# Performance work log

Measured on AMD Instinct MI355X. Metric: run time of the kernel, lower is better.

## Reference

```python
import jax, jax.numpy as jnp
import numpy as np

B, T, I, H = 256, 512, 300, 128


def setup_inputs() -> dict:
    key = jax.random.key(0)
    ks = jax.random.split(key, 7)
    s_ih = 1.0 / np.sqrt(H)
    return {
        "x": jax.random.normal(ks[0], (B, T, I), dtype=jnp.float32),
        # PyTorch LSTM params, gate order i,f,g,o stacked along first axis
        "W_ih": jax.random.uniform(ks[1], (4 * H, I), minval=-s_ih, maxval=s_ih, dtype=jnp.float32),
        "W_hh": jax.random.uniform(ks[2], (4 * H, H), minval=-s_ih, maxval=s_ih, dtype=jnp.float32),
        "b_ih": jax.random.uniform(ks[3], (4 * H,), minval=-s_ih, maxval=s_ih, dtype=jnp.float32),
        "b_hh": jax.random.uniform(ks[4], (4 * H,), minval=-s_ih, maxval=s_ih, dtype=jnp.float32),
        "fc_w": jax.random.uniform(ks[5], (1, H), minval=-s_ih, maxval=s_ih, dtype=jnp.float32),
        "fc_b": jax.random.uniform(ks[6], (1,), minval=-s_ih, maxval=s_ih, dtype=jnp.float32),
    }


def _lstm_last_h(x, W_ih, W_hh, b_ih, b_hh):
    # Precompute input contributions for all timesteps at once: [B,T,4H]
    xg = jnp.einsum("bti,gi->btg", x, W_ih) + b_ih + b_hh
    xg = jnp.transpose(xg, (1, 0, 2))  # [T,B,4H] for scan

    def step(carry, xg_t):
        h, c = carry
        gates = xg_t + h @ W_hh.T  # [B,4H]
        i, f, g, o = jnp.split(gates, 4, axis=-1)
        i = jax.nn.sigmoid(i)
        f = jax.nn.sigmoid(f)
        g = jnp.tanh(g)
        o = jax.nn.sigmoid(o)
        c = f * c + i * g
        h = o * jnp.tanh(c)
        return (h, c), None

    h0 = jnp.zeros((x.shape[0], W_hh.shape[1]), dtype=x.dtype)
    (h_last, _), _ = jax.lax.scan(step, (h0, h0), xg)
    return h_last  # [B,H]


def reference(x, W_ih, W_hh, b_ih, b_hh, fc_w, fc_b):
    h_last = _lstm_last_h(x, W_ih, W_hh, b_ih, b_hh)
    return h_last @ fc_w.T + fc_b  # [B,1]
```

## Files before the change

### kernel.cpp

```cpp
#include <hip/hip_runtime.h>
#include <cstdint>
#include <cstddef>

#define Bb   256
#define Tt   512
#define Ii   300
#define Hh   128
#define G4   512
#define KP   320
#define Mm   (Bb*Tt)

typedef _Float16 h2v   __attribute__((ext_vector_type(2)));
typedef _Float16 half8 __attribute__((ext_vector_type(8)));
typedef float    f32x4 __attribute__((ext_vector_type(4)));

static __device__ __forceinline__ h2v as_h2(unsigned int u){ union{unsigned int u; h2v h;} c; c.u=u; return c.h; }
static __device__ __forceinline__ unsigned int as_u32(h2v h){ union{unsigned int u; h2v h;} c; c.h=h; return c.u; }

#if __has_builtin(__builtin_amdgcn_fdot2)
#define FDOT2(a,b,c) __builtin_amdgcn_fdot2((a),(b),(c),false)
#else
static __device__ __forceinline__ float FDOT2(h2v a, h2v b, float c){
  return c + (float)a[0]*(float)b[0] + (float)a[1]*(float)b[1];
}
#endif

__global__ __launch_bounds__(256) void conv_x(const float* __restrict__ x, unsigned int* __restrict__ x16){
  int idx = blockIdx.x*256 + threadIdx.x;
  int r   = idx / 160;
  int kk2 = idx - r*160;
  int kk  = kk2*2;
  const float* xr = x + (size_t)r*Ii;
  float v0 = (kk   < Ii) ? xr[kk]   : 0.f;
  float v1 = (kk+1 < Ii) ? xr[kk+1] : 0.f;
  h2v h; h[0] = (_Float16)v0; h[1] = (_Float16)v1;
  x16[idx] = as_u32(h);
}

__global__ __launch_bounds__(256) void conv_small(const float* __restrict__ Wih, const float* __restrict__ Whh,
      const float* __restrict__ bih, const float* __restrict__ bhh,
      unsigned int* __restrict__ W16, unsigned int* __restrict__ Whh2, float* __restrict__ bias){
  int idx = blockIdx.x*256 + threadIdx.x;
  if (idx < G4*160){
    int r = idx/160, kk2 = idx - r*160, kk = kk2*2;
    const float* wr = Wih + (size_t)r*Ii;
    float v0 = (kk   < Ii) ? wr[kk]   : 0.f;
    float v1 = (kk+1 < Ii) ? wr[kk+1] : 0.f;
    h2v h; h[0]=(_Float16)v0; h[1]=(_Float16)v1;
    W16[idx] = as_u32(h);
  } else if (idx < G4*160 + G4*64){
    int t = idx - G4*160; int j = t>>6, kk = t&63;
    float v0 = Whh[j*Hh + kk*2], v1 = Whh[j*Hh + kk*2 + 1];
    h2v h; h[0]=(_Float16)v0; h[1]=(_Float16)v1;
    Whh2[t] = as_u32(h);
  } else if (idx < G4*160 + G4*64 + G4){
    int d = idx - (G4*160 + G4*64);
    bias[d] = bih[d] + bhh[d];
  }
}

__global__ __launch_bounds__(256,2) void gemm16(const _Float16* __restrict__ A, const _Float16* __restrict__ Bm,
       const float* __restrict__ bias, float* __restrict__ C){
  __shared__ _Float16 As[128][32];
  __shared__ _Float16 Bs[128][32];
  int tid = threadIdx.x;
  int w = tid>>6, lane = tid&63;
  int bm = blockIdx.x*128, bn = blockIdx.y*128;
  f32x4 acc[2][8];
  #pragma unroll
  for (int i=0;i<2;i++)
    #pragma unroll
    for (int j=0;j<8;j++) acc[i][j] = (f32x4){0.f,0.f,0.f,0.f};

  int srow = tid>>1, scol = (tid&1)*16;
  const uint4* ga = (const uint4*)(A  + (size_t)(bm+srow)*KP + scol);
  const uint4* gb = (const uint4*)(Bm + (size_t)(bn+srow)*KP + scol);

  int q = lane>>4, mr = lane&15;
  int m0 = w*32;

  for (int kt=0; kt<KP/32; ++kt){
    __syncthreads();
    uint4 va0 = ga[0], va1 = ga[1];
    uint4 vb0 = gb[0], vb1 = gb[1];
    *(uint4*)&As[srow][scol]   = va0; *(uint4*)&As[srow][scol+8] = va1;
    *(uint4*)&Bs[srow][scol]   = vb0; *(uint4*)&Bs[srow][scol+8] = vb1;
    ga += 4; gb += 4;
    __syncthreads();
    half8 af0 = *(const half8*)&As[m0 + mr][q*8];
    half8 af1 = *(const half8*)&As[m0 + 16 + mr][q*8];
    #pragma unroll
    for (int j=0;j<8;j++){
      half8 bf = *(const half8*)&Bs[j*16 + mr][q*8];
      acc[0][j] = __builtin_amdgcn_mfma_f32_16x16x32_f16(af0, bf, acc[0][j], 0,0,0);
      acc[1][j] = __builtin_amdgcn_mfma_f32_16x16x32_f16(af1, bf, acc[1][j], 0,0,0);
    }
  }
  #pragma unroll
  for (int j=0;j<8;j++){
    int gc = bn + j*16 + mr;
    float bv = bias[gc];
    #pragma unroll
    for (int i=0;i<2;i++){
      int gr0 = bm + w*32 + i*16 + q*4;
      #pragma unroll
      for (int reg=0; reg<4; ++reg)
        C[(size_t)(gr0+reg)*G4 + gc] = acc[i][j][reg] + bv;
    }
  }
}

__global__ __launch_bounds__(256,1) void lstm_rec(const float* __restrict__ xg, const unsigned int* __restrict__ Whh2,
     const float* __restrict__ fcw, const float* __restrict__ fcb, float* __restrict__ out){
  int tid = threadIdx.x;
  int b = blockIdx.x;
  h2v w0[64], w1[64];
  #pragma unroll
  for (int kk=0; kk<64; ++kk){
    w0[kk] = as_h2(Whh2[tid*64 + kk]);
    w1[kk] = as_h2(Whh2[(tid+256)*64 + kk]);
  }
  __shared__ __align__(16) unsigned short hsh[128];
  __shared__ float2 fo_sh[128];
  __shared__ float red[256];
  if (tid < 128) hsh[tid] = 0;
  float creg = 0.f, hreg = 0.f;
  const float* xrow = xg + (size_t)b * (Tt*G4);
  float xc0 = xrow[tid], xc1 = xrow[256+tid];
  __syncthreads();

  for (int t=0; t<Tt; ++t){
    float xn0 = 0.f, xn1 = 0.f;
    if (t < Tt-1){ const float* xr = xrow + (size_t)(t+1)*G4; xn0 = xr[tid]; xn1 = xr[256+tid]; }
    float a0 = xc0, a1 = xc1;
    const uint4* hv = (const uint4*)hsh;
    #pragma unroll
    for (int kq=0; kq<16; ++kq){
      uint4 hq = hv[kq];
      h2v p0 = as_h2(hq.x), p1 = as_h2(hq.y), p2 = as_h2(hq.z), p3 = as_h2(hq.w);
      a0 = FDOT2(p0, w0[kq*4+0], a0); a1 = FDOT2(p0, w1[kq*4+0], a1);
      a0 = FDOT2(p1, w0[kq*4+1], a0); a1 = FDOT2(p1, w1[kq*4+1], a1);
      a0 = FDOT2(p2, w0[kq*4+2], a0); a1 = FDOT2(p2, w1[kq*4+2], a1);
      a0 = FDOT2(p3, w0[kq*4+3], a0); a1 = FDOT2(p3, w1[kq*4+3], a1);
    }
    if (tid >= 128){
      float f = 1.f/(1.f+__expf(-a0));
      float o = 1.f/(1.f+__expf(-a1));
      fo_sh[tid-128] = make_float2(f,o);
    }
    __syncthreads();
    if (tid < 128){
      float ig = 1.f/(1.f+__expf(-a0));
      float eg = __expf(2.f*a1); float g = 1.f - 2.f/(eg+1.f);
      float2 fo = fo_sh[tid];
      creg = fo.x*creg + ig*g;
      float ec = __expf(2.f*creg); float tc = 1.f - 2.f/(ec+1.f);
      hreg = fo.y*tc;
      union { _Float16 f; unsigned short s; } cv; cv.f = (_Float16)hreg;
      hsh[tid] = cv.s;
    }
    __syncthreads();
    xc0 = xn0; xc1 = xn1;
  }

  red[tid] = (tid < 128) ? hreg*fcw[tid] : 0.f;
  __syncthreads();
  for (int s=128; s>=1; s>>=1){
    if (tid < s) red[tid] += red[tid+s];
    __syncthreads();
  }
  if (tid == 0) out[b] = red[0] + fcb[0];
}

extern "C" void kernel_launch(void* const* d_in, const int* in_sizes, int n_in,
                              void* d_out, int out_size, void* d_ws, size_t ws_size,
                              hipStream_t stream){
  const float* x   = (const float*)d_in[0];
  const float* Wih = (const float*)d_in[1];
  const float* Whh = (const float*)d_in[2];
  const float* bih = (const float*)d_in[3];
  const float* bhh = (const float*)d_in[4];
  const float* fcw = (const float*)d_in[5];
  const float* fcb = (const float*)d_in[6];
  float* out = (float*)d_out;
  char* ws = (char*)d_ws;

  unsigned int* x16   = (unsigned int*)(ws);
  unsigned int* W16   = (unsigned int*)(ws + 83886080);
  unsigned int* Whh2w = (unsigned int*)(ws + 84213760);
  float*        bias  = (float*)      (ws + 84344832);
  float*        xg    = (float*)      (ws + 84346880);

  hipLaunchKernelGGL(conv_x,     dim3(81920),  dim3(256), 0, stream, x, x16);
  hipLaunchKernelGGL(conv_small, dim3(450),    dim3(256), 0, stream, Wih, Whh, bih, bhh, W16, Whh2w, bias);
  hipLaunchKernelGGL(gemm16,     dim3(1024,4), dim3(256), 0, stream,
                     (const _Float16*)x16, (const _Float16*)W16, bias, xg);
  hipLaunchKernelGGL(lstm_rec,   dim3(256),    dim3(256), 0, stream, xg, Whh2w, fcw, fcb, out);
}
```

Before: 708.0 us.

## Use one thread per gate row in LSTM recurrence with 512-thread blocks

```diff
diff --git a/kernel.cpp b/kernel.cpp
--- a/kernel.cpp
+++ b/kernel.cpp
@@ -110,62 +110,59 @@
   }
 }
 
-__global__ __launch_bounds__(256,1) void lstm_rec(const float* __restrict__ xg, const unsigned int* __restrict__ Whh2,
+__global__ __launch_bounds__(512,2) void lstm_rec(const float* __restrict__ xg, const unsigned int* __restrict__ Whh2,
      const float* __restrict__ fcw, const float* __restrict__ fcb, float* __restrict__ out){
   int tid = threadIdx.x;
   int b = blockIdx.x;
-  h2v w0[64], w1[64];
+  int d = tid & 127, g = tid >> 7;
+  h2v w[64];
   #pragma unroll
-  for (int kk=0; kk<64; ++kk){
-    w0[kk] = as_h2(Whh2[tid*64 + kk]);
-    w1[kk] = as_h2(Whh2[(tid+256)*64 + kk]);
-  }
+  for (int kk=0; kk<64; ++kk) w[kk] = as_h2(Whh2[tid*64 + kk]);
+
   __shared__ __align__(16) unsigned short hsh[128];
-  __shared__ float2 fo_sh[128];
-  __shared__ float red[256];
+  __shared__ __align__(16) float gsh[512];
+  __shared__ float red[128];
   if (tid < 128) hsh[tid] = 0;
   float creg = 0.f, hreg = 0.f;
   const float* xrow = xg + (size_t)b * (Tt*G4);
-  float xc0 = xrow[tid], xc1 = xrow[256+tid];
+  float xc = xrow[tid];
   __syncthreads();
 
   for (int t=0; t<Tt; ++t){
-    float xn0 = 0.f, xn1 = 0.f;
-    if (t < Tt-1){ const float* xr = xrow + (size_t)(t+1)*G4; xn0 = xr[tid]; xn1 = xr[256+tid]; }
-    float a0 = xc0, a1 = xc1;
+    float xn = 0.f;
+    if (t < Tt-1) xn = xrow[(size_t)(t+1)*G4 + tid];
+    float a0 = xc, a1 = 0.f;
     const uint4* hv = (const uint4*)hsh;
     #pragma unroll
-    for (int kq=0; kq<16; ++kq){
-      uint4 hq = hv[kq];
-      h2v p0 = as_h2(hq.x), p1 = as_h2(hq.y), p2 = as_h2(hq.z), p3 = as_h2(hq.w);
-      a0 = FDOT2(p0, w0[kq*4+0], a0); a1 = FDOT2(p0, w1[kq*4+0], a1);
-      a0 = FDOT2(p1, w0[kq*4+1], a0); a1 = FDOT2(p1, w1[kq*4+1], a1);
-      a0 = FDOT2(p2, w0[kq*4+2], a0); a1 = FDOT2(p2, w1[kq*4+2], a1);
-      a0 = FDOT2(p3, w0[kq*4+3], a0); a1 = FDOT2(p3, w1[kq*4+3], a1);
+    for (int kq=0; kq<8; ++kq){
+      uint4 hq0 = hv[kq*2], hq1 = hv[kq*2+1];
+      a0 = FDOT2(as_h2(hq0.x), w[kq*8+0], a0); a1 = FDOT2(as_h2(hq0.y), w[kq*8+1], a1);
+      a0 = FDOT2(as_h2(hq0.z), w[kq*8+2], a0); a1 = FDOT2(as_h2(hq0.w), w[kq*8+3], a1);
+      a0 = FDOT2(as_h2(hq1.x), w[kq*8+4], a0); a1 = FDOT2(as_h2(hq1.y), w[kq*8+5], a1);
+      a0 = FDOT2(as_h2(hq1.z), w[kq*8+6], a0); a1 = FDOT2(as_h2(hq1.w), w[kq*8+7], a1);
     }
-    if (tid >= 128){
-      float f = 1.f/(1.f+__expf(-a0));
-      float o = 1.f/(1.f+__expf(-a1));
-      fo_sh[tid-128] = make_float2(f,o);
+    float a = a0 + a1;
+    float act;
+    if (g == 2){ float e = __expf(2.f*a); act = 1.f - 2.f/(e+1.f); }
+    else       { act = 1.f/(1.f+__expf(-a)); }
+    gsh[d*4+g] = act;
+    __syncthreads();
+    float4 gv = *(const float4*)&gsh[d*4];
+    creg = gv.y*creg + gv.x*gv.z;
+    float ec = __expf(2.f*creg); float tc = 1.f - 2.f/(ec+1.f);
+    hreg = gv.w*tc;
+    if (g == 0){
+      union{ _Float16 f; unsigned short s; } cv; cv.f = (_Float16)hreg;
+      hsh[d] = cv.s;
     }
     __syncthreads();
-    if (tid < 128){
-      float ig = 1.f/(1.f+__expf(-a0));
-      float eg = __expf(2.f*a1); float g = 1.f - 2.f/(eg+1.f);
-      float2 fo = fo_sh[tid];
-      creg = fo.x*creg + ig*g;
-      float ec = __expf(2.f*creg); float tc = 1.f - 2.f/(ec+1.f);
-      hreg = fo.y*tc;
-      union { _Float16 f; unsigned short s; } cv; cv.f = (_Float16)hreg;
-      hsh[tid] = cv.s;
-    }
-    __syncthreads();
-    xc0 = xn0; xc1 = xn1;
+    xc = xn;
   }
 
-  red[tid] = (tid < 128) ? hreg*fcw[tid] : 0.f;
+  if (tid < 128) red[tid] = hreg * fcw[tid];
   __syncthreads();
-  for (int s=128; s>=1; s>>=1){
+  #pragma unroll
+  for (int s=64; s>=1; s>>=1){
     if (tid < s) red[tid] += red[tid+s];
     __syncthreads();
   }
@@ -195,5 +192,5 @@
   hipLaunchKernelGGL(conv_small, dim3(450),    dim3(256), 0, stream, Wih, Whh, bih, bhh, W16, Whh2w, bias);
   hipLaunchKernelGGL(gemm16,     dim3(1024,4), dim3(256), 0, stream,
                      (const _Float16*)x16, (const _Float16*)W16, bias, xg);
-  hipLaunchKernelGGL(lstm_rec,   dim3(256),    dim3(256), 0, stream, xg, Whh2w, fcw, fcb, out);
+  hipLaunchKernelGGL(lstm_rec,   dim3(256),    dim3(512), 0, stream, xg, Whh2w, fcw, fcb, out);
 }
```

New measurement: 661.8 us. 6.5% less time.
